# Performance work log

Hardware: AMD Instinct MI355X
Metric: run time of the kernel (lower is better)

## Reference

```python
import jax, jax.numpy as jnp
import numpy as np

DIM = 1024
HEADS = 16
DIM_HEAD = 64
INNER = HEADS * DIM_HEAD
B, M, N = 8, 4096, 256
EPS = 1e-5


def layer_norm(x, g, b):
    mu = jnp.mean(x, axis=-1, keepdims=True)
    var = jnp.mean(jnp.square(x - mu), axis=-1, keepdims=True)
    return (x - mu) * jax.lax.rsqrt(var + EPS) * g + b


def setup_inputs() -> dict:
    key = jax.random.key(0)
    ks = jax.random.split(key, 8)
    x = jax.random.normal(ks[0], (B, M, DIM), dtype=jnp.float32)
    latents = jax.random.normal(ks[1], (B, N, DIM), dtype=jnp.float32)
    x_att_mask = jax.random.randint(ks[2], (B, M), 0, 2) == 1  # True = masked
    s = 0.02
    Wq = jax.random.normal(ks[3], (DIM, INNER), dtype=jnp.float32) * s
    Wkv = jax.random.normal(ks[4], (DIM, 2 * INNER), dtype=jnp.float32) * s
    Wo = jax.random.normal(ks[5], (INNER, DIM), dtype=jnp.float32) * s
    return {
        "x": x, "latents": latents, "x_att_mask": x_att_mask,
        "nm_g": jnp.ones((DIM,), jnp.float32), "nm_b": jnp.zeros((DIM,), jnp.float32),
        "nl_g": jnp.ones((DIM,), jnp.float32), "nl_b": jnp.zeros((DIM,), jnp.float32),
        "Wq": Wq, "Wkv": Wkv, "Wo": Wo,
    }


def reference(x, latents, x_att_mask, nm_g, nm_b, nl_g, nl_b, Wq, Wkv, Wo):
    b, n, d = latents.shape
    h, dh = HEADS, DIM_HEAD
    scale = dh ** (-0.5)

    # additive mask: concat(media mask, all-False latent mask); True -> -inf, False -> +1 (faithful quirk)
    latent_mask = jnp.zeros((b, n), dtype=bool)
    full_mask = jnp.concatenate([x_att_mask, latent_mask], axis=1)  # [b, m+n]
    add_mask = jnp.where(full_mask, -jnp.inf, 1.0).astype(x.dtype)[:, None, None, :]  # [b,1,1,m+n]

    xn = layer_norm(x, nm_g, nm_b)
    ln = layer_norm(latents, nl_g, nl_b)

    q = (ln @ Wq).reshape(b, n, h, dh).transpose(0, 2, 1, 3)  # bhnd
    kv_in = jnp.concatenate([xn, ln], axis=1)                 # [b, m+n, d]
    kv = kv_in @ Wkv
    k, v = jnp.split(kv, 2, axis=-1)
    j = kv_in.shape[1]
    k = k.reshape(b, j, h, dh).transpose(0, 2, 1, 3)
    v = v.reshape(b, j, h, dh).transpose(0, 2, 1, 3)

    sim = jnp.einsum('bhid,bhjd->bhij', q * scale, k)
    sim = sim - jnp.max(sim, axis=-1, keepdims=True)
    sim = sim + add_mask
    attn = jax.nn.softmax(sim, axis=-1)
    out = jnp.einsum('bhij,bhjd->bhid', attn, v)
    out = out.transpose(0, 2, 1, 3).reshape(b, n, h * dh)
    return out @ Wo
```

## Files before the change

### kernel.cpp

```cpp
#include <hip/hip_runtime.h>
#include <hip/hip_bf16.h>
#include <stdint.h>

#define HEADS 16
#define DH    64
#define NB    8
#define MQ    256
#define MX    4096
#define JD    4352
#define DIMV  1024

typedef __bf16 bf16;
typedef __bf16 bf16x8 __attribute__((ext_vector_type(8)));
typedef float  f32x4  __attribute__((ext_vector_type(4)));

#define SWZ(r, c) (((c) ^ ((r) & 7)))

__device__ __forceinline__ void gl_lds16(const void* g, void* l) {
  __builtin_amdgcn_global_load_lds((const __attribute__((address_space(1))) void*)g,
                                   (__attribute__((address_space(3))) void*)l, 16, 0, 0);
}

__global__ __launch_bounds__(256) void ln_kernel(
    const float* __restrict__ X, const float* __restrict__ gw, const float* __restrict__ bw,
    bf16* __restrict__ out_kv, bf16* __restrict__ out_ln, int is_lat)
{
  const int row = blockIdx.x;
  const int tid = threadIdx.x;
  const float4 v = ((const float4*)(X + (size_t)row * DIMV))[tid];
  float s  = v.x + v.y + v.z + v.w;
  float s2 = v.x*v.x + v.y*v.y + v.z*v.z + v.w*v.w;
#pragma unroll
  for (int m = 1; m < 64; m <<= 1) { s += __shfl_xor(s, m); s2 += __shfl_xor(s2, m); }
  __shared__ float red[8];
  const int wid = tid >> 6;
  if ((tid & 63) == 0) { red[wid*2] = s; red[wid*2+1] = s2; }
  __syncthreads();
  s  = red[0] + red[2] + red[4] + red[6];
  s2 = red[1] + red[3] + red[5] + red[7];
  const float mu  = s * (1.0f / DIMV);
  const float var = s2 * (1.0f / DIMV) - mu * mu;
  const float rst = rsqrtf(var + 1e-5f);
  const float4 g4 = ((const float4*)gw)[tid];
  const float4 b4 = ((const float4*)bw)[tid];
  union { bf16 h[4]; short4 s4; } u;
  u.h[0] = (bf16)((v.x - mu) * rst * g4.x + b4.x);
  u.h[1] = (bf16)((v.y - mu) * rst * g4.y + b4.y);
  u.h[2] = (bf16)((v.z - mu) * rst * g4.z + b4.z);
  u.h[3] = (bf16)((v.w - mu) * rst * g4.w + b4.w);
  size_t kvrow;
  if (is_lat) { int b = row >> 8;  int i = row & 255;  kvrow = (size_t)b * JD + MX + i; }
  else        { int b = row >> 12; int j = row & 4095; kvrow = (size_t)b * JD + j; }
  *(short4*)(out_kv + kvrow * DIMV + tid * 4) = u.s4;
  if (is_lat) *(short4*)(out_ln + (size_t)row * DIMV + tid * 4) = u.s4;
}

__global__ __launch_bounds__(256) void transpose_w(
    const float* __restrict__ in, bf16* __restrict__ out, int R, int C)
{
  __shared__ float t[64][65];
  const int tilesC = C >> 6;
  const int tc = blockIdx.x % tilesC, tr = blockIdx.x / tilesC;
  const int r0 = tr << 6, c0 = tc << 6;
  const int lr = threadIdx.x >> 4;
  const int lc = (threadIdx.x & 15) << 2;
#pragma unroll
  for (int p = 0; p < 4; p++) {
    float4 v = *(const float4*)&in[(size_t)(r0 + lr + p*16) * C + c0 + lc];
    t[lr + p*16][lc    ] = v.x; t[lr + p*16][lc + 1] = v.y;
    t[lr + p*16][lc + 2] = v.z; t[lr + p*16][lc + 3] = v.w;
  }
  __syncthreads();
#pragma unroll
  for (int p = 0; p < 4; p++) {
    const int oc = lr + p*16;
    union { bf16 h[4]; short4 s4; } u;
    u.h[0] = (bf16)t[lc    ][oc]; u.h[1] = (bf16)t[lc + 1][oc];
    u.h[2] = (bf16)t[lc + 2][oc]; u.h[3] = (bf16)t[lc + 3][oc];
    *(short4*)&out[(size_t)(c0 + oc) * R + r0 + lc] = u.s4;
  }
}

__global__ __launch_bounds__(256) void mask_detect(
    const unsigned char* __restrict__ m, int n, int* __restrict__ flag)
{
  const int tid = threadIdx.x;
  int cnt = 0;
  for (int i = tid; i < n; i += 256) cnt += (m[i] != 0) ? 1 : 0;
#pragma unroll
  for (int mm = 1; mm < 64; mm <<= 1) cnt += __shfl_xor(cnt, mm);
  __shared__ int r4[4];
  if ((tid & 63) == 0) r4[tid >> 6] = cnt;
  __syncthreads();
  if (tid == 0) {
    int t = r4[0] + r4[1] + r4[2] + r4[3];
    flag[0] = (t * 16 > n * 5) ? 1 : 0;
  }
}

__global__ __launch_bounds__(256) void mask_build(
    const void* __restrict__ mraw, const int* __restrict__ flag, float* __restrict__ mm)
{
  const int idx = blockIdx.x * 256 + threadIdx.x;
  const int b = idx / JD, j = idx - b * JD;
  float v = 1.0f;
  if (j < MX) {
    bool masked = (*flag) ? (((const unsigned char*)mraw)[b * MX + j] != 0)
                          : (((const int*)mraw)[b * MX + j] != 0);
    v = masked ? 0.0f : 1.0f;
  }
  mm[idx] = v;
}

__global__ __launch_bounds__(512, 2) void gemm256(
    const bf16* __restrict__ A, const bf16* __restrict__ Bt,
    bf16* __restrict__ outR, bf16* __restrict__ outVT,
    int K, int kSplitX)
{
  __shared__ bf16 sm[65536];

  const int tid = threadIdx.x;
  const int lane = tid & 63, wid = tid >> 6;
  const int wr = wid >> 2, wc = wid & 3;
  const int lc = lane & 15, lq = lane >> 4;
  const int srow = tid >> 3, sc = tid & 7;
  const int ssw = SWZ(srow, sc) * 8;

  int bid = blockIdx.y * gridDim.x + blockIdx.x;
  const int nwg = gridDim.x * gridDim.y;
  bid = (bid & 7) * (nwg >> 3) + (bid >> 3);
  const int bx = bid % gridDim.x;
  const int by = bid / gridDim.x;

  const bool vmode = (bx >= kSplitX);
  const int n0 = vmode ? 1024 + (bx - kSplitX) * 256 : bx * 256;
  const int m0 = by * 256;

  const bf16* Arow = vmode ? (Bt + (size_t)n0 * K) : (A + (size_t)m0 * K);
  const bf16* Brow = vmode ? (A + (size_t)m0 * K) : (Bt + (size_t)n0 * K);
  const bf16* Abase = Arow + (size_t)srow * K + ssw;
  const bf16* Bbase = Brow + (size_t)srow * K + ssw;

  auto stageA = [&](int cbuf, int h, int kt) {
    gl_lds16(Abase + (size_t)(h*128     ) * K + (size_t)kt * 64,
             &sm[cbuf*16384 + (h*128     )*64 + tid*8]);
    gl_lds16(Abase + (size_t)(h*128 + 64) * K + (size_t)kt * 64,
             &sm[cbuf*16384 + (h*128 + 64)*64 + tid*8]);
  };
  auto stageB = [&](int cbuf, int h, int kt) {
    gl_lds16(Bbase + (size_t)(h*128     ) * K + (size_t)kt * 64,
             &sm[32768 + cbuf*16384 + (h*128     )*64 + tid*8]);
    gl_lds16(Bbase + (size_t)(h*128 + 64) * K + (size_t)kt * 64,
             &sm[32768 + cbuf*16384 + (h*128 + 64)*64 + tid*8]);
  };

  f32x4 acc[8][4];
#pragma unroll
  for (int i = 0; i < 8; i++)
#pragma unroll
    for (int j = 0; j < 4; j++)
#pragma unroll
      for (int r = 0; r < 4; r++) acc[i][j][r] = 0.f;

  const int NT = K >> 6;

  stageA(0, 0, 0); stageA(0, 1, 0);
  stageB(0, 0, 0); stageB(0, 1, 0);
  stageA(1, 0, 1); stageA(1, 1, 1);
  asm volatile("s_waitcnt vmcnt(4)" ::: "memory");
  __builtin_amdgcn_s_barrier();

  for (int kt = 0; kt < NT; ++kt) {
    const int c = kt & 1;
    const bf16* As = sm + c * 16384;
    const bf16* Bs = sm + 32768 + c * 16384;
    const bool st = (kt + 1 < NT);
    bf16x8 bfrag[4][2];
#pragma unroll
    for (int p = 0; p < 4; ++p) {
      bf16x8 afrag[2][2];
#pragma unroll
      for (int mi = 0; mi < 2; ++mi)
#pragma unroll
        for (int kk = 0; kk < 2; ++kk)
          afrag[mi][kk] = *(const bf16x8*)&As[(wr*128 + (p*2 + mi)*16 + lc)*64 + SWZ(lc, kk*4 + lq)*8];
      if (p == 0) {
#pragma unroll
        for (int n = 0; n < 4; ++n)
#pragma unroll
          for (int kk = 0; kk < 2; ++kk)
            bfrag[n][kk] = *(const bf16x8*)&Bs[(wc*64 + n*16 + lc)*64 + SWZ(lc, kk*4 + lq)*8];
        if (st) stageB(1 - c, 0, kt + 1);
      }
      if (p == 1 && st) stageB(1 - c, 1, kt + 1);
      __builtin_amdgcn_s_barrier();
      __builtin_amdgcn_s_setprio(1);
#pragma unroll
      for (int kk = 0; kk < 2; ++kk)
#pragma unroll
        for (int mi = 0; mi < 2; ++mi)
#pragma unroll
          for (int n = 0; n < 4; ++n)
            acc[p*2 + mi][n] = __builtin_amdgcn_mfma_f32_16x16x32_bf16(
                afrag[mi][kk], bfrag[n][kk], acc[p*2 + mi][n], 0, 0, 0);
      __builtin_amdgcn_s_setprio(0);
      __builtin_amdgcn_s_barrier();
    }
    if (kt + 2 < NT) {
      stageA(c, 0, kt + 2);
      stageA(c, 1, kt + 2);
      asm volatile("s_waitcnt vmcnt(4)" ::: "memory");
      __builtin_amdgcn_s_barrier();
    } else if (kt + 1 < NT) {
      asm volatile("s_waitcnt vmcnt(0)" ::: "memory");
      __builtin_amdgcn_s_barrier();
    }
  }

  __syncthreads();
  bf16* Ct = sm;
#pragma unroll
  for (int m = 0; m < 8; ++m)
#pragma unroll
    for (int n = 0; n < 4; ++n) {
      const int col = wc*64 + n*16 + lc;
      const int cch = col >> 3, cw = col & 7;
#pragma unroll
      for (int r = 0; r < 4; ++r) {
        const int row = wr*128 + m*16 + lq*4 + r;
        Ct[row*256 + (((cch ^ (row & 31)) << 3) + cw)] = (bf16)acc[m][n][r];
      }
    }
  __syncthreads();

  const int cch = tid & 31, r0 = tid >> 5;
  if (!vmode) {
#pragma unroll
    for (int i = 0; i < 16; ++i) {
      const int row = r0 + i*16;
      bf16x8 v = *(const bf16x8*)&Ct[row*256 + ((cch ^ (row & 31)) << 3)];
      *(bf16x8*)(outR + (size_t)(m0 + row) * 1024 + n0 + cch*8) = v;
    }
  } else {
    const int bb = m0 / JD;
    const int jbase = m0 - bb * JD;
#pragma unroll
    for (int i = 0; i < 16; ++i) {
      const int row = r0 + i*16;
      const int cc = n0 + row - 1024;
      bf16x8 v = *(const bf16x8*)&Ct[row*256 + ((cch ^ (row & 31)) << 3)];
      bf16* dst = outVT + (((size_t)(bb*HEADS + (cc >> 6)))*64 + (cc & 63)) * JD
                        + jbase + cch*8;
      *(bf16x8*)dst = v;
    }
  }
}

__global__ __launch_bounds__(256) void gemm128(
    const bf16* __restrict__ A, const bf16* __restrict__ Bt,
    float* __restrict__ Cf, bf16* __restrict__ outR, bf16* __restrict__ outVT,
    int N, int K, int kSplitX, int mode)
{
  __shared__ bf16 smem[2 * 128 * 64];
  bf16* As = smem;
  bf16* Bs = smem + 128 * 64;
  bf16* Ct = smem;

  const int tid = threadIdx.x;
  const int lane = tid & 63, wid = tid >> 6;
  const int wr = wid >> 1, wc = wid & 1;
  const int bx = blockIdx.x;
  const int m0 = blockIdx.y * 128;
  const bool vmode = (mode == 1) && (bx >= kSplitX);
  const int n0 = vmode ? 1024 + (bx - kSplitX) * 128 : bx * 128;
  const int srow = tid >> 3, sc = tid & 7;
  const int ssw = SWZ(srow, sc) * 8;
  const int lc = lane & 15, lq = lane >> 4;

  f32x4 acc[4][4];
#pragma unroll
  for (int i = 0; i < 4; i++)
#pragma unroll
    for (int j = 0; j < 4; j++)
#pragma unroll
      for (int r = 0; r < 4; r++) acc[i][j][r] = 0.f;

  const bf16* Arow = vmode ? (Bt + (size_t)n0 * K) : (A + (size_t)m0 * K);
  const bf16* Brow = vmode ? (A + (size_t)m0 * K) : (Bt + (size_t)n0 * K);
  const bf16* Abase = Arow + (size_t)srow * K + ssw;
  const bf16* Bbase = Brow + (size_t)srow * K + ssw;

  for (int k0 = 0; k0 < K; k0 += 64) {
    __syncthreads();
#pragma unroll
    for (int q = 0; q < 4; q++) {
      gl_lds16(Abase + (size_t)q * 32 * K + k0, &As[(srow + q*32) * 64 + sc*8]);
      gl_lds16(Bbase + (size_t)q * 32 * K + k0, &Bs[(srow + q*32) * 64 + sc*8]);
    }
    asm volatile("s_waitcnt vmcnt(0)" ::: "memory");
    __syncthreads();
#pragma unroll
    for (int kk = 0; kk < 2; kk++) {
      bf16x8 af[4], bfr[4];
#pragma unroll
      for (int mi = 0; mi < 4; mi++)
        af[mi] = *(const bf16x8*)&As[(wr*64 + mi*16 + lc) * 64 + SWZ(lc, kk*4 + lq)*8];
#pragma unroll
      for (int ni = 0; ni < 4; ni++)
        bfr[ni] = *(const bf16x8*)&Bs[(wc*64 + ni*16 + lc) * 64 + SWZ(lc, kk*4 + lq)*8];
#pragma unroll
      for (int mi = 0; mi < 4; mi++)
#pragma unroll
        for (int ni = 0; ni < 4; ni++)
          acc[mi][ni] = __builtin_amdgcn_mfma_f32_16x16x32_bf16(af[mi], bfr[ni], acc[mi][ni], 0, 0, 0);
    }
  }

  if (mode == 0) {
#pragma unroll
    for (int mi = 0; mi < 4; mi++)
#pragma unroll
      for (int ni = 0; ni < 4; ni++) {
        const int r = m0 + wr*64 + mi*16 + lq*4;
        const int c = n0 + wc*64 + ni*16 + lc;
#pragma unroll
        for (int reg = 0; reg < 4; reg++)
          Cf[(size_t)(r + reg) * N + c] = acc[mi][ni][reg];
      }
    return;
  }

  __syncthreads();
#pragma unroll
  for (int mi = 0; mi < 4; mi++)
#pragma unroll
    for (int ni = 0; ni < 4; ni++) {
      const int col = wc*64 + ni*16 + lc;
      const int cch = col >> 3, cw = col & 7;
#pragma unroll
      for (int reg = 0; reg < 4; reg++) {
        const int row = wr*64 + mi*16 + lq*4 + reg;
        Ct[row*128 + ((cch ^ (row & 15)) << 3) + cw] = (bf16)acc[mi][ni][reg];
      }
    }
  __syncthreads();

  const int cch = tid & 15, r0 = tid >> 4;
  {
    bf16* dst0 = outR + (size_t)m0 * 1024 + n0 + cch*8;
#pragma unroll
    for (int i = 0; i < 8; i++) {
      const int row = r0 + i*16;
      bf16x8 v = *(const bf16x8*)&Ct[row*128 + ((cch ^ r0) << 3)];
      *(bf16x8*)(dst0 + (size_t)row * 1024) = v;
    }
  }
}

__global__ __launch_bounds__(512) void attn_kernel(
    const bf16* __restrict__ Qrows,
    const bf16* __restrict__ Krows,
    const bf16* __restrict__ VT,
    const float* __restrict__ mmul,
    bf16* __restrict__ outp)
{
  const int bh = blockIdx.x >> 1, qt = blockIdx.x & 1;
  const int b = bh >> 4, h = bh & 15;
  __shared__ bf16 Qs[128 * 64];
  __shared__ bf16 Ks[64 * 64];
  __shared__ bf16 VTs[64 * 64];
  __shared__ bf16 Ps[8][16 * 64];
  const int tid = threadIdx.x, lane = tid & 63, w = tid >> 6;
  const int lc = lane & 15, lq = lane >> 4;
  const int srow = tid >> 3, sc = tid & 7;
  const int ssw = SWZ(srow, sc) * 8;

  const bf16* Qg = Qrows + ((size_t)(b*MQ + qt*128)) * 1024 + h*64;
  const bf16* Kg = Krows + ((size_t)b * JD) * 1024 + h*64;
  const bf16* Vg = VT + ((size_t)bh * 64) * JD;

  gl_lds16(Qg + (size_t)srow * 1024 + ssw, &Qs[tid*8]);
  gl_lds16(Qg + (size_t)(srow + 64) * 1024 + ssw, &Qs[(tid + 512)*8]);
  asm volatile("s_waitcnt vmcnt(0)" ::: "memory");
  __syncthreads();

  bf16x8 qf[2];
#pragma unroll
  for (int kk = 0; kk < 2; kk++)
    qf[kk] = *(const bf16x8*)&Qs[(w*16 + lc) * 64 + SWZ(lc, kk*4 + lq)*8];

  f32x4 oacc[4];
  float den[4];
#pragma unroll
  for (int di = 0; di < 4; di++)
#pragma unroll
    for (int r = 0; r < 4; r++) oacc[di][r] = 0.f;
#pragma unroll
  for (int r = 0; r < 4; r++) den[r] = 0.f;

  for (int j0 = 0; j0 < JD; j0 += 64) {
    __syncthreads();
    gl_lds16(Kg + (size_t)(j0 + srow) * 1024 + ssw, &Ks[tid*8]);
    gl_lds16(Vg + (size_t)srow * JD + j0 + ssw, &VTs[tid*8]);
    asm volatile("s_waitcnt vmcnt(0)" ::: "memory");
    __syncthreads();

    f32x4 sacc[4];
#pragma unroll
    for (int nj = 0; nj < 4; nj++)
#pragma unroll
      for (int r = 0; r < 4; r++) sacc[nj][r] = 0.f;
#pragma unroll
    for (int kk = 0; kk < 2; kk++) {
      bf16x8 kf[4];
#pragma unroll
      for (int nj = 0; nj < 4; nj++)
        kf[nj] = *(const bf16x8*)&Ks[(nj*16 + lc) * 64 + SWZ(lc, kk*4 + lq)*8];
#pragma unroll
      for (int nj = 0; nj < 4; nj++)
        sacc[nj] = __builtin_amdgcn_mfma_f32_16x16x32_bf16(qf[kk], kf[nj], sacc[nj], 0, 0, 0);
    }

#pragma unroll
    for (int nj = 0; nj < 4; nj++) {
      const float mm = mmul[b * JD + j0 + nj*16 + lc];
#pragma unroll
      for (int r = 0; r < 4; r++) {
        const float p = exp2f(sacc[nj][r] * 0.18033688f) * mm;
        den[r] += p;
        const int row = lq*4 + r, col = nj*16 + lc;
        Ps[w][row*64 + (((col >> 3) ^ (row & 7)) << 3) + (col & 7)] = (bf16)p;
      }
    }

#pragma unroll
    for (int kk = 0; kk < 2; kk++) {
      bf16x8 pf = *(const bf16x8*)&Ps[w][lc*64 + SWZ(lc, kk*4 + lq)*8];
#pragma unroll
      for (int di = 0; di < 4; di++) {
        bf16x8 vf = *(const bf16x8*)&VTs[(di*16 + lc) * 64 + SWZ(lc, kk*4 + lq)*8];
        oacc[di] = __builtin_amdgcn_mfma_f32_16x16x32_bf16(pf, vf, oacc[di], 0, 0, 0);
      }
    }
  }

#pragma unroll
  for (int r = 0; r < 4; r++) {
    float d = den[r];
    d += __shfl_xor(d, 1); d += __shfl_xor(d, 2);
    d += __shfl_xor(d, 4); d += __shfl_xor(d, 8);
    den[r] = 1.0f / d;
  }

#pragma unroll
  for (int di = 0; di < 4; di++) {
    const int col = h*64 + di*16 + lc;
#pragma unroll
    for (int r = 0; r < 4; r++) {
      const int i = qt*128 + w*16 + lq*4 + r;
      outp[(size_t)(b*MQ + i) * 1024 + col] = (bf16)(oacc[di][r] * den[r]);
    }
  }
}

extern "C" void kernel_launch(void* const* d_in, const int* in_sizes, int n_in,
                              void* d_out, int out_size, void* d_ws, size_t ws_size,
                              hipStream_t stream)
{
  const float* x    = (const float*)d_in[0];
  const float* lat  = (const float*)d_in[1];
  const void*  mraw = d_in[2];
  const float* nm_g = (const float*)d_in[3];
  const float* nm_b = (const float*)d_in[4];
  const float* nl_g = (const float*)d_in[5];
  const float* nl_b = (const float*)d_in[6];
  const float* Wq   = (const float*)d_in[7];
  const float* Wkv  = (const float*)d_in[8];
  const float* Wo   = (const float*)d_in[9];
  float* out = (float*)d_out;

  char* p = (char*)d_ws;
  auto alloc = [&](size_t bytes) { char* r = p; p += (bytes + 255) & ~(size_t)255; return r; };

  bf16*  kv_in  = (bf16*)alloc((size_t)NB * JD * DIMV * 2);
  bf16*  Krows  = (bf16*)alloc((size_t)NB * JD * 1024 * 2);
  bf16*  VTbuf  = (bf16*)alloc((size_t)NB * HEADS * 64 * JD * 2);
  bf16*  WqT    = (bf16*)alloc((size_t)1024 * 1024 * 2);
  bf16*  WkvT   = (bf16*)alloc((size_t)2048 * 1024 * 2);
  bf16*  WoT    = (bf16*)alloc((size_t)1024 * 1024 * 2);
  bf16*  ln_buf = (bf16*)alloc((size_t)NB * MQ * DIMV * 2);
  bf16*  Qrows  = (bf16*)alloc((size_t)NB * MQ * 1024 * 2);
  bf16*  attout = (bf16*)alloc((size_t)NB * MQ * DIMV * 2);
  float* mmulp  = (float*)alloc((size_t)NB * JD * 4);
  int*   flag   = (int*)alloc(256);
  (void)ws_size; (void)in_sizes; (void)n_in; (void)out_size;

  ln_kernel<<<NB * MX, 256, 0, stream>>>(x,   nm_g, nm_b, kv_in, nullptr, 0);
  ln_kernel<<<NB * MQ, 256, 0, stream>>>(lat, nl_g, nl_b, kv_in, ln_buf, 1);
  transpose_w<<<256, 256, 0, stream>>>(Wq,  WqT,  1024, 1024);
  transpose_w<<<512, 256, 0, stream>>>(Wkv, WkvT, 1024, 2048);
  transpose_w<<<256, 256, 0, stream>>>(Wo,  WoT,  1024, 1024);
  mask_detect<<<1, 256, 0, stream>>>((const unsigned char*)mraw, 32768, flag);
  mask_build<<<136, 256, 0, stream>>>(mraw, flag, mmulp);

  gemm256<<<dim3(8, 136), 512, 0, stream>>>(kv_in, WkvT, Krows, VTbuf, 1024, 4);
  gemm128<<<dim3(8, 16), 256, 0, stream>>>(ln_buf, WqT, nullptr, Qrows, nullptr,
                                           1024, 1024, 8, 1);
  attn_kernel<<<256, 512, 0, stream>>>(Qrows, Krows, VTbuf, mmulp, attout);
  gemm128<<<dim3(8, 16), 256, 0, stream>>>(attout, WoT, out, nullptr, nullptr,
                                           1024, 1024, 8, 0);
}
```

Before: 571.7 us.

## Deepen GEMM B-tile prefetch to two stages and halve inner-loop phases

Restructures the main bf16 GEMM k-loop so that both the A and B tiles are prefetched two iterations ahead into the double buffer. Previously B was only one iteration ahead. The loop goes from four phases of two 16-row A fragments each to two phases of four fragments, which halves the barrier count per k-step. The vmcnt waits are updated to match the larger number of outstanding loads. The aim is to hide global-to-LDS latency and cut synchronisation, at the cost of more live fragment registers and more in-flight loads.

```diff
diff --git a/kernel.cpp b/kernel.cpp
--- a/kernel.cpp
+++ b/kernel.cpp
@@ -141,17 +141,17 @@
   const bf16* Abase = Arow + (size_t)srow * K + ssw;
   const bf16* Bbase = Brow + (size_t)srow * K + ssw;
 
-  auto stageA = [&](int cbuf, int h, int kt) {
-    gl_lds16(Abase + (size_t)(h*128     ) * K + (size_t)kt * 64,
-             &sm[cbuf*16384 + (h*128     )*64 + tid*8]);
-    gl_lds16(Abase + (size_t)(h*128 + 64) * K + (size_t)kt * 64,
-             &sm[cbuf*16384 + (h*128 + 64)*64 + tid*8]);
+  auto stageA = [&](int cbuf, int kt) {
+#pragma unroll
+    for (int h = 0; h < 4; ++h)
+      gl_lds16(Abase + (size_t)(h*64) * K + (size_t)kt * 64,
+               &sm[cbuf*16384 + (h*64)*64 + tid*8]);
   };
-  auto stageB = [&](int cbuf, int h, int kt) {
-    gl_lds16(Bbase + (size_t)(h*128     ) * K + (size_t)kt * 64,
-             &sm[32768 + cbuf*16384 + (h*128     )*64 + tid*8]);
-    gl_lds16(Bbase + (size_t)(h*128 + 64) * K + (size_t)kt * 64,
-             &sm[32768 + cbuf*16384 + (h*128 + 64)*64 + tid*8]);
+  auto stageB = [&](int cbuf, int kt) {
+#pragma unroll
+    for (int h = 0; h < 4; ++h)
+      gl_lds16(Bbase + (size_t)(h*64) * K + (size_t)kt * 64,
+               &sm[32768 + cbuf*16384 + (h*64)*64 + tid*8]);
   };
 
   f32x4 acc[8][4];
@@ -164,55 +164,69 @@
 
   const int NT = K >> 6;
 
-  stageA(0, 0, 0); stageA(0, 1, 0);
-  stageB(0, 0, 0); stageB(0, 1, 0);
-  stageA(1, 0, 1); stageA(1, 1, 1);
-  asm volatile("s_waitcnt vmcnt(4)" ::: "memory");
+  stageB(0, 0); stageA(0, 0);
+  stageB(1, 1); stageA(1, 1);
+  asm volatile("s_waitcnt vmcnt(8)" ::: "memory");
   __builtin_amdgcn_s_barrier();
 
   for (int kt = 0; kt < NT; ++kt) {
     const int c = kt & 1;
     const bf16* As = sm + c * 16384;
     const bf16* Bs = sm + 32768 + c * 16384;
-    const bool st = (kt + 1 < NT);
+    const bool st = (kt + 2 < NT);
+
     bf16x8 bfrag[4][2];
-#pragma unroll
-    for (int p = 0; p < 4; ++p) {
-      bf16x8 afrag[2][2];
-#pragma unroll
-      for (int mi = 0; mi < 2; ++mi)
-#pragma unroll
-        for (int kk = 0; kk < 2; ++kk)
-          afrag[mi][kk] = *(const bf16x8*)&As[(wr*128 + (p*2 + mi)*16 + lc)*64 + SWZ(lc, kk*4 + lq)*8];
-      if (p == 0) {
+    bf16x8 af0[4][2];
+#pragma unroll
+    for (int mi = 0; mi < 4; ++mi)
+#pragma unroll
+      for (int kk = 0; kk < 2; ++kk)
+        af0[mi][kk] = *(const bf16x8*)&As[(wr*128 + mi*16 + lc)*64 + SWZ(lc, kk*4 + lq)*8];
+#pragma unroll
+    for (int n = 0; n < 4; ++n)
+#pragma unroll
+      for (int kk = 0; kk < 2; ++kk)
+        bfrag[n][kk] = *(const bf16x8*)&Bs[(wc*64 + n*16 + lc)*64 + SWZ(lc, kk*4 + lq)*8];
+    __builtin_amdgcn_s_barrier();
+    __builtin_amdgcn_s_setprio(1);
+#pragma unroll
+    for (int kk = 0; kk < 2; ++kk)
+#pragma unroll
+      for (int mi = 0; mi < 4; ++mi)
 #pragma unroll
         for (int n = 0; n < 4; ++n)
-#pragma unroll
-          for (int kk = 0; kk < 2; ++kk)
-            bfrag[n][kk] = *(const bf16x8*)&Bs[(wc*64 + n*16 + lc)*64 + SWZ(lc, kk*4 + lq)*8];
-        if (st) stageB(1 - c, 0, kt + 1);
+          acc[mi][n] = __builtin_amdgcn_mfma_f32_16x16x32_bf16(
+              af0[mi][kk], bfrag[n][kk], acc[mi][n], 0, 0, 0);
+    __builtin_amdgcn_s_setprio(0);
+    __builtin_amdgcn_s_barrier();
+
+    bf16x8 af1[4][2];
+#pragma unroll
+    for (int mi = 0; mi < 4; ++mi)
+#pragma unroll
+      for (int kk = 0; kk < 2; ++kk)
+        af1[mi][kk] = *(const bf16x8*)&As[(wr*128 + (mi+4)*16 + lc)*64 + SWZ(lc, kk*4 + lq)*8];
+    if (st) stageB(c, kt + 2);
+    __builtin_amdgcn_s_barrier();
+    __builtin_amdgcn_s_setprio(1);
+#pragma unroll
+    for (int kk = 0; kk < 2; ++kk)
+#pragma unroll
+      for (int mi = 0; mi < 4; ++mi)
+#pragma unroll
+        for (int n = 0; n < 4; ++n)
+          acc[mi+4][n] = __builtin_amdgcn_mfma_f32_16x16x32_bf16(
+              af1[mi][kk], bfrag[n][kk], acc[mi+4][n], 0, 0, 0);
+    __builtin_amdgcn_s_setprio(0);
+    __builtin_amdgcn_s_barrier();
+
+    if (kt + 1 < NT) {
+      if (st) {
+        stageA(c, kt + 2);
+        asm volatile("s_waitcnt vmcnt(8)" ::: "memory");
+      } else {
+        asm volatile("s_waitcnt vmcnt(0)" ::: "memory");
       }
-      if (p == 1 && st) stageB(1 - c, 1, kt + 1);
-      __builtin_amdgcn_s_barrier();
-      __builtin_amdgcn_s_setprio(1);
-#pragma unroll
-      for (int kk = 0; kk < 2; ++kk)
-#pragma unroll
-        for (int mi = 0; mi < 2; ++mi)
-#pragma unroll
-          for (int n = 0; n < 4; ++n)
-            acc[p*2 + mi][n] = __builtin_amdgcn_mfma_f32_16x16x32_bf16(
-                afrag[mi][kk], bfrag[n][kk], acc[p*2 + mi][n], 0, 0, 0);
-      __builtin_amdgcn_s_setprio(0);
-      __builtin_amdgcn_s_barrier();
-    }
-    if (kt + 2 < NT) {
-      stageA(c, 0, kt + 2);
-      stageA(c, 1, kt + 2);
-      asm volatile("s_waitcnt vmcnt(4)" ::: "memory");
-      __builtin_amdgcn_s_barrier();
-    } else if (kt + 1 < NT) {
-      asm volatile("s_waitcnt vmcnt(0)" ::: "memory");
       __builtin_amdgcn_s_barrier();
     }
   }
```

Result: no change. 573.8 us (+0.4%).
